# Kernel tuning notes

Hardware: AMD Instinct MI355X
Metric: run time of the kernel (lower is better)

## Reference

```python
import jax, jax.numpy as jnp
import numpy as np

NUM_CHUNKS = 8
TOP_K = 2
IN_F = 4096
HID_F = 4096
OUT_F = 4096
B = 4096


def setup_inputs() -> dict:
    key = jax.random.key(0)
    k = jax.random.split(key, 5)
    cin = IN_F // NUM_CHUNKS    # 512
    cout = HID_F // NUM_CHUNKS  # 512
    s_in = 1.0 / np.sqrt(cin)
    s_fin = 1.0 / np.sqrt(cout * TOP_K)
    return {
        "x": jax.random.normal(k[0], (B, IN_F), dtype=jnp.float32),
        # stacked chunk-expert Linear params: y = x @ W + b
        "W_chunks": jax.random.uniform(k[1], (NUM_CHUNKS, cin, cout), jnp.float32, -s_in, s_in),
        "b_chunks": jax.random.uniform(k[2], (NUM_CHUNKS, cout), jnp.float32, -s_in, s_in),
        "W_final": jax.random.uniform(k[3], (cout * TOP_K, OUT_F), jnp.float32, -s_fin, s_fin),
        "b_final": jax.random.uniform(k[4], (OUT_F,), jnp.float32, -s_fin, s_fin),
    }


def reference(x, W_chunks, b_chunks, W_final, b_final):
    Bsz = x.shape[0]
    # split into chunks along feature dim: (B, num_chunks, chunk_in)
    xr = x.reshape(Bsz, NUM_CHUNKS, -1)
    # per-chunk activity = mean(|chunk|) over the whole batch (matches torch .abs().mean())
    activities = jnp.mean(jnp.abs(xr), axis=(0, 2))  # (num_chunks,)
    _, topk_idx = jax.lax.top_k(activities, TOP_K)    # descending, like torch.topk
    # gather selected chunks and their expert weights, run small GEMMs
    x_sel = xr[:, topk_idx, :]                        # (B, k, chunk_in)
    h = jnp.einsum('bkc,kcd->bkd', x_sel, W_chunks[topk_idx]) + b_chunks[topk_idx]
    h = h.reshape(Bsz, -1)                            # concat along feature dim
    out = h @ W_final + b_final                       # (B, out_features)
    return out
```

## Files before the change

kernel.cpp:

```cpp
#include <hip/hip_runtime.h>


typedef __bf16 bf16x8_t __attribute__((ext_vector_type(8)));
typedef float  f32x4_t  __attribute__((ext_vector_type(4)));

__device__ inline unsigned short f2bf(float f) {
    __bf16 b = (__bf16)f;
    return __builtin_bit_cast(unsigned short, b);
}


__device__ inline void stage_glds(const unsigned short* gtile, int stride, int row0,
                                  unsigned short* lds, int lane) {
    const int r8 = lane >> 3;
    const int gg = (lane & 7) ^ r8;
    const unsigned short* gp = gtile + (size_t)(row0 + r8) * stride + gg * 8;
    unsigned short* lp = lds + row0 * 64;
    __builtin_amdgcn_global_load_lds((const __attribute__((address_space(1))) void*)gp,
                                     (__attribute__((address_space(3))) void*)lp,
                                     16, 0, 0);
}

__device__ inline bf16x8_t ldsfrag(const unsigned short* Ls, int row, int kb) {
    return *(const bf16x8_t*)(Ls + row * 64 + (((kb >> 3) ^ (row & 7)) * 8));
}

__global__ void activity_kernel(const float* __restrict__ x, float* __restrict__ part) {
    const int chunk = blockIdx.y;
    const int tid = threadIdx.x;
    const int colf4 = tid & 127;
    const int rsub = tid >> 7;
    const float4* base = (const float4*)x + (size_t)chunk * 128 + colf4;
    float s = 0.f;
    #pragma unroll 4
    for (int i = 0; i < 32; ++i) {
        int row = blockIdx.x * 64 + i * 2 + rsub;
        float4 v = base[(size_t)row * 1024];
        s += fabsf(v.x) + fabsf(v.y) + fabsf(v.z) + fabsf(v.w);
    }
    #pragma unroll
    for (int off = 32; off > 0; off >>= 1) s += __shfl_down(s, off, 64);
    __shared__ float wsum[4];
    if ((tid & 63) == 0) wsum[tid >> 6] = s;
    __syncthreads();
    if (tid == 0) part[chunk * 64 + blockIdx.x] = wsum[0] + wsum[1] + wsum[2] + wsum[3];
}

__global__ void topk_kernel(const float* __restrict__ part, int* __restrict__ idx) {
    __shared__ float act[8];
    const int lane = threadIdx.x & 63;
    const int wave = threadIdx.x >> 6;
    float s = part[wave * 64 + lane];
    #pragma unroll
    for (int off = 32; off > 0; off >>= 1) s += __shfl_down(s, off, 64);
    if (lane == 0) act[wave] = s;
    __syncthreads();
    if (threadIdx.x == 0) {
        float v0 = -1e30f, v1 = -1e30f; int b0 = 0, b1 = 0;
        for (int i = 0; i < 8; ++i) {
            float v = act[i];
            if (v > v0) { v1 = v0; b1 = b0; v0 = v; b0 = i; }
            else if (v > v1) { v1 = v; b1 = i; }
        }
        idx[0] = b0; idx[1] = b1;
    }
}

__global__ void transpose_cvt_kernel(const float* __restrict__ src, unsigned short* __restrict__ dst,
                                     int R, int C, const int* __restrict__ idx, int chunk_elems) {
    if (idx) { src += (size_t)idx[blockIdx.z] * chunk_elems; dst += (size_t)blockIdx.z * chunk_elems; }
    __shared__ float tile[32][33];
    const int tx = threadIdx.x, ty = threadIdx.y;
    const int cb = blockIdx.x * 32, rb = blockIdx.y * 32;
    #pragma unroll
    for (int i = 0; i < 4; ++i)
        tile[ty + i * 8][tx] = src[(size_t)(rb + ty + i * 8) * C + cb + tx];
    __syncthreads();
    #pragma unroll
    for (int i = 0; i < 4; ++i)
        dst[(size_t)(cb + ty + i * 8) * R + rb + tx] = f2bf(tile[tx][ty + i * 8]);
}

__global__ __launch_bounds__(256, 2)
void gemm1_kernel(const float* __restrict__ x, const unsigned short* __restrict__ wct,
                  const float* __restrict__ bc, const int* __restrict__ idx,
                  unsigned short* __restrict__ h) {
    const int z = blockIdx.z;
    const int idxz = idx[z];
    const int m0 = blockIdx.x * 64;
    const int n0 = blockIdx.y * 64;

    __shared__ unsigned short As[64 * 64];
    __shared__ unsigned short Bs[64 * 64];

    const int tid = threadIdx.x;
    const int wave = tid >> 6;
    const int lane = tid & 63;
    const int wm = (wave >> 1) * 32;
    const int wn = (wave & 1) * 32;
    const int rl = lane & 15;
    const int quad = lane >> 4;

    const float* xtile = x + (size_t)m0 * 4096 + idxz * 512;
    const unsigned short* bttile = wct + (size_t)z * 512 * 512 + (size_t)n0 * 512;

    f32x4_t acc[2][2] = {};

    const int ar = tid >> 2;
    const int aq = tid & 3;

    for (int k0 = 0; k0 < 512; k0 += 64) {
        #pragma unroll
        for (int s = wave; s < 8; s += 4)
            stage_glds(bttile + k0, 512, s * 8, Bs, lane);
        const float* gr = xtile + (size_t)ar * 4096 + k0;
        #pragma unroll
        for (int j = 0; j < 2; ++j) {
            int gg = aq * 2 + j;
            float4 a = *(const float4*)(gr + gg * 8);
            float4 b = *(const float4*)(gr + gg * 8 + 4);
            bf16x8_t v;
            v[0] = (__bf16)a.x; v[1] = (__bf16)a.y; v[2] = (__bf16)a.z; v[3] = (__bf16)a.w;
            v[4] = (__bf16)b.x; v[5] = (__bf16)b.y; v[6] = (__bf16)b.z; v[7] = (__bf16)b.w;
            *(bf16x8_t*)(As + ar * 64 + ((gg ^ (ar & 7)) * 8)) = v;
        }
        __syncthreads();
        #pragma unroll
        for (int kq = 0; kq < 2; ++kq) {
            const int kb = kq * 32 + quad * 8;
            bf16x8_t af[2], bfr[2];
            #pragma unroll
            for (int i = 0; i < 2; ++i) {
                af[i]  = ldsfrag(As, wm + i * 16 + rl, kb);
                bfr[i] = ldsfrag(Bs, wn + i * 16 + rl, kb);
            }
            #pragma unroll
            for (int mi = 0; mi < 2; ++mi)
                #pragma unroll
                for (int ni = 0; ni < 2; ++ni)
                    acc[mi][ni] = __builtin_amdgcn_mfma_f32_16x16x32_bf16(af[mi], bfr[ni], acc[mi][ni], 0, 0, 0);
        }
        __syncthreads();
    }

    const int row_l = quad * 4;
    const float* bias = bc + (size_t)idxz * 512;
    #pragma unroll
    for (int ni = 0; ni < 2; ++ni) {
        int col = n0 + wn + ni * 16 + rl;
        float bv = bias[col];
        #pragma unroll
        for (int mi = 0; mi < 2; ++mi) {
            #pragma unroll
            for (int j = 0; j < 4; ++j) {
                int row = m0 + wm + mi * 16 + row_l + j;
                h[(size_t)row * 1024 + z * 512 + col] = f2bf(acc[mi][ni][j] + bv);
            }
        }
    }
}

__global__ __launch_bounds__(256, 2)
void gemm2_kernel(const unsigned short* __restrict__ A, const unsigned short* __restrict__ Bt,
                  const float* __restrict__ bias, float* __restrict__ C) {
    const int m0 = blockIdx.x * 128;
    const int n0 = blockIdx.y * 128;

    __shared__ unsigned short As[128 * 64];
    __shared__ unsigned short Bs[128 * 64];

    const int tid = threadIdx.x;
    const int wave = tid >> 6;
    const int lane = tid & 63;
    const int wm = (wave >> 1) * 64;
    const int wn = (wave & 1) * 64;
    const int rl = lane & 15;
    const int quad = lane >> 4;

    const unsigned short* Atile = A + (size_t)m0 * 1024;
    const unsigned short* Btile = Bt + (size_t)n0 * 1024;

    f32x4_t acc[4][4] = {};

    for (int k0 = 0; k0 < 1024; k0 += 64) {
        #pragma unroll
        for (int s = wave; s < 32; s += 4) {
            if (s < 16) stage_glds(Atile + k0, 1024, s * 8, As, lane);
            else        stage_glds(Btile + k0, 1024, (s - 16) * 8, Bs, lane);
        }
        __syncthreads();
        #pragma unroll
        for (int kq = 0; kq < 2; ++kq) {
            const int kb = kq * 32 + quad * 8;
            bf16x8_t af[4], bfr[4];
            #pragma unroll
            for (int i = 0; i < 4; ++i) {
                af[i]  = ldsfrag(As, wm + i * 16 + rl, kb);
                bfr[i] = ldsfrag(Bs, wn + i * 16 + rl, kb);
            }
            #pragma unroll
            for (int mi = 0; mi < 4; ++mi)
                #pragma unroll
                for (int ni = 0; ni < 4; ++ni)
                    acc[mi][ni] = __builtin_amdgcn_mfma_f32_16x16x32_bf16(af[mi], bfr[ni], acc[mi][ni], 0, 0, 0);
        }
        __syncthreads();
    }

    const int row_l = quad * 4;
    float bv[4];
    #pragma unroll
    for (int ni = 0; ni < 4; ++ni) bv[ni] = bias[n0 + wn + ni * 16 + rl];
    #pragma unroll
    for (int mi = 0; mi < 4; ++mi) {
        #pragma unroll
        for (int ni = 0; ni < 4; ++ni) {
            int col = n0 + wn + ni * 16 + rl;
            #pragma unroll
            for (int j = 0; j < 4; ++j) {
                int row = m0 + wm + mi * 16 + row_l + j;
                C[(size_t)row * 4096 + col] = acc[mi][ni][j] + bv[ni];
            }
        }
    }
}

extern "C" void kernel_launch(void* const* d_in, const int* in_sizes, int n_in,
                              void* d_out, int out_size, void* d_ws, size_t ws_size,
                              hipStream_t stream) {
    const float* x    = (const float*)d_in[0];
    const float* Wc   = (const float*)d_in[1];
    const float* bc   = (const float*)d_in[2];
    const float* Wf   = (const float*)d_in[3];
    const float* bfin = (const float*)d_in[4];
    float* out = (float*)d_out;

    float* part = (float*)d_ws;
    int*   idx  = (int*)((char*)d_ws + 2048);
    unsigned short* h   = (unsigned short*)((char*)d_ws + 4096);
    unsigned short* wct = h   + (size_t)4096 * 1024;
    unsigned short* wft = wct + (size_t)2 * 512 * 512;

    activity_kernel<<<dim3(64, 8), 256, 0, stream>>>(x, part);
    topk_kernel<<<1, 512, 0, stream>>>(part, idx);
    transpose_cvt_kernel<<<dim3(16, 16, 2), dim3(32, 8), 0, stream>>>(Wc, wct, 512, 512, idx, 512 * 512);
    transpose_cvt_kernel<<<dim3(128, 32, 1), dim3(32, 8), 0, stream>>>(Wf, wft, 1024, 4096, nullptr, 0);

    gemm1_kernel<<<dim3(64, 8, 2), 256, 0, stream>>>(x, wct, bc, idx, h);
    gemm2_kernel<<<dim3(32, 32, 1), 256, 0, stream>>>(h, wft, bfin, out);
}
```

Measured before the change: 193.1 us.

## Fuse all stages into one cooperative persistent kernel with grid syncs

```diff
diff --git a/kernel.cpp b/kernel.cpp
--- a/kernel.cpp
+++ b/kernel.cpp
@@ -1,4 +1,7 @@
 #include <hip/hip_runtime.h>
+#include <hip/hip_cooperative_groups.h>
+
+namespace cg = cooperative_groups;
 
 
 typedef __bf16 bf16x8_t __attribute__((ext_vector_type(8)));
@@ -8,7 +11,6 @@
     __bf16 b = (__bf16)f;
     return __builtin_bit_cast(unsigned short, b);
 }
-
 
 __device__ inline void stage_glds(const unsigned short* gtile, int stride, int row0,
                                   unsigned short* lds, int lane) {
@@ -23,6 +25,248 @@
 
 __device__ inline bf16x8_t ldsfrag(const unsigned short* Ls, int row, int kb) {
     return *(const bf16x8_t*)(Ls + row * 64 + (((kb >> 3) ^ (row & 7)) * 8));
+}
+
+__device__ inline void gemm1_tile(const float* __restrict__ x, const unsigned short* __restrict__ wct,
+                                  const float* __restrict__ bc, unsigned short* __restrict__ h,
+                                  int z, int idxz, int m0, int n0,
+                                  unsigned short* As, unsigned short* Bs,
+                                  int tid, int wave, int lane) {
+    const int wm = (wave >> 1) * 32;
+    const int wn = (wave & 1) * 32;
+    const int rl = lane & 15;
+    const int quad = lane >> 4;
+    const float* xtile = x + (size_t)m0 * 4096 + idxz * 512;
+    const unsigned short* bttile = wct + (size_t)z * 262144 + (size_t)n0 * 512;
+
+    f32x4_t acc[2][2] = {};
+    const int ar = tid >> 2;
+    const int aq = tid & 3;
+
+    for (int k0 = 0; k0 < 512; k0 += 64) {
+        #pragma unroll
+        for (int s = wave; s < 8; s += 4)
+            stage_glds(bttile + k0, 512, s * 8, Bs, lane);
+        const float* gr = xtile + (size_t)ar * 4096 + k0;
+        #pragma unroll
+        for (int j = 0; j < 2; ++j) {
+            int gg = aq * 2 + j;
+            float4 a = *(const float4*)(gr + gg * 8);
+            float4 c = *(const float4*)(gr + gg * 8 + 4);
+            bf16x8_t v;
+            v[0] = (__bf16)a.x; v[1] = (__bf16)a.y; v[2] = (__bf16)a.z; v[3] = (__bf16)a.w;
+            v[4] = (__bf16)c.x; v[5] = (__bf16)c.y; v[6] = (__bf16)c.z; v[7] = (__bf16)c.w;
+            *(bf16x8_t*)(As + ar * 64 + ((gg ^ (ar & 7)) * 8)) = v;
+        }
+        __syncthreads();
+        #pragma unroll
+        for (int kq = 0; kq < 2; ++kq) {
+            const int kb = kq * 32 + quad * 8;
+            bf16x8_t af[2], bfr[2];
+            #pragma unroll
+            for (int i = 0; i < 2; ++i) {
+                af[i]  = ldsfrag(As, wm + i * 16 + rl, kb);
+                bfr[i] = ldsfrag(Bs, wn + i * 16 + rl, kb);
+            }
+            #pragma unroll
+            for (int mi = 0; mi < 2; ++mi)
+                #pragma unroll
+                for (int ni = 0; ni < 2; ++ni)
+                    acc[mi][ni] = __builtin_amdgcn_mfma_f32_16x16x32_bf16(af[mi], bfr[ni], acc[mi][ni], 0, 0, 0);
+        }
+        __syncthreads();
+    }
+
+    const int row_l = quad * 4;
+    const float* bias = bc + (size_t)idxz * 512;
+    #pragma unroll
+    for (int ni = 0; ni < 2; ++ni) {
+        int col = n0 + wn + ni * 16 + rl;
+        float bv = bias[col];
+        #pragma unroll
+        for (int mi = 0; mi < 2; ++mi) {
+            #pragma unroll
+            for (int j = 0; j < 4; ++j) {
+                int row = m0 + wm + mi * 16 + row_l + j;
+                h[(size_t)row * 1024 + z * 512 + col] = f2bf(acc[mi][ni][j] + bv);
+            }
+        }
+    }
+}
+
+__device__ inline void gemm2_tile(const unsigned short* __restrict__ h, const unsigned short* __restrict__ wft,
+                                  const float* __restrict__ bfin, float* __restrict__ out,
+                                  int m0, int n0, unsigned short* As, unsigned short* Bs,
+                                  int wave, int lane) {
+    const int wm = (wave >> 1) * 64;
+    const int wn = (wave & 1) * 64;
+    const int rl = lane & 15;
+    const int quad = lane >> 4;
+    const unsigned short* Atile = h + (size_t)m0 * 1024;
+    const unsigned short* Btile = wft + (size_t)n0 * 1024;
+
+    f32x4_t acc[4][4] = {};
+
+    for (int k0 = 0; k0 < 1024; k0 += 64) {
+        #pragma unroll
+        for (int s = wave; s < 32; s += 4) {
+            if (s < 16) stage_glds(Atile + k0, 1024, s * 8, As, lane);
+            else        stage_glds(Btile + k0, 1024, (s - 16) * 8, Bs, lane);
+        }
+        __syncthreads();
+        #pragma unroll
+        for (int kq = 0; kq < 2; ++kq) {
+            const int kb = kq * 32 + quad * 8;
+            bf16x8_t af[4], bfr[4];
+            #pragma unroll
+            for (int i = 0; i < 4; ++i) {
+                af[i]  = ldsfrag(As, wm + i * 16 + rl, kb);
+                bfr[i] = ldsfrag(Bs, wn + i * 16 + rl, kb);
+            }
+            #pragma unroll
+            for (int mi = 0; mi < 4; ++mi)
+                #pragma unroll
+                for (int ni = 0; ni < 4; ++ni)
+                    acc[mi][ni] = __builtin_amdgcn_mfma_f32_16x16x32_bf16(af[mi], bfr[ni], acc[mi][ni], 0, 0, 0);
+        }
+        __syncthreads();
+    }
+
+    const int row_l = quad * 4;
+    float bv[4];
+    #pragma unroll
+    for (int ni = 0; ni < 4; ++ni) bv[ni] = bfin[n0 + wn + ni * 16 + rl];
+    #pragma unroll
+    for (int mi = 0; mi < 4; ++mi) {
+        #pragma unroll
+        for (int ni = 0; ni < 4; ++ni) {
+            int col = n0 + wn + ni * 16 + rl;
+            #pragma unroll
+            for (int j = 0; j < 4; ++j) {
+                int row = m0 + wm + mi * 16 + row_l + j;
+                out[(size_t)row * 4096 + col] = acc[mi][ni][j] + bv[ni];
+            }
+        }
+    }
+}
+
+__global__ __launch_bounds__(256, 2)
+void mega_kernel(const float* __restrict__ x, const float* __restrict__ Wc,
+                 const float* __restrict__ bc, const float* __restrict__ Wf,
+                 const float* __restrict__ bfin, float* __restrict__ out,
+                 float* __restrict__ part, int* __restrict__ idxg,
+                 unsigned short* __restrict__ h, unsigned short* __restrict__ wct,
+                 unsigned short* __restrict__ wft) {
+    cg::grid_group grid = cg::this_grid();
+    __shared__ __align__(16) unsigned char lds_raw[32 * 1024];
+
+    const int b = blockIdx.x;
+    const int tid = threadIdx.x;
+    const int wave = tid >> 6;
+    const int lane = tid & 63;
+
+    {
+        const int chunk = b & 7;
+        const int rg = b >> 3;
+        const int colf4 = tid & 127;
+        const int rsub = tid >> 7;
+        const float4* base = (const float4*)x + (size_t)chunk * 128 + colf4;
+        float s = 0.f;
+        #pragma unroll 4
+        for (int i = 0; i < 32; ++i) {
+            int row = rg * 64 + i * 2 + rsub;
+            float4 v = base[(size_t)row * 1024];
+            s += fabsf(v.x) + fabsf(v.y) + fabsf(v.z) + fabsf(v.w);
+        }
+        #pragma unroll
+        for (int off = 32; off > 0; off >>= 1) s += __shfl_down(s, off, 64);
+        float* wsum = (float*)lds_raw;
+        if (lane == 0) wsum[wave] = s;
+        __syncthreads();
+        if (tid == 0) part[chunk * 64 + rg] = wsum[0] + wsum[1] + wsum[2] + wsum[3];
+    }
+    __threadfence();
+    grid.sync();
+
+    if (b == 0) {
+        float* red = (float*)lds_raw;
+        float* act8 = (float*)(lds_raw + 1024);
+        const int c = tid >> 5, j = tid & 31;
+        red[tid] = part[c * 64 + j] + part[c * 64 + j + 32];
+        __syncthreads();
+        if (tid < 8) {
+            float a = 0.f;
+            for (int k = 0; k < 32; ++k) a += red[tid * 32 + k];
+            act8[tid] = a;
+        }
+        __syncthreads();
+        if (tid == 0) {
+            float v0 = -1e30f, v1 = -1e30f; int b0 = 0, b1 = 0;
+            for (int i = 0; i < 8; ++i) {
+                float v = act8[i];
+                if (v > v0) { v1 = v0; b1 = b0; v0 = v; b0 = i; }
+                else if (v > v1) { v1 = v; b1 = i; }
+            }
+            idxg[0] = b0; idxg[1] = b1;
+        }
+    }
+    __threadfence();
+    grid.sync();
+
+    const int sel0 = ((volatile int*)idxg)[0];
+    const int sel1 = ((volatile int*)idxg)[1];
+
+    {
+        float (*tile)[33] = (float (*)[33])lds_raw;
+        const int tx = tid & 31, ty = tid >> 5;
+        for (int j = b; j < 4608; j += 512) {
+            const float* src; unsigned short* dst; int R, C, cb, rb;
+            if (j < 4096) {
+                src = Wf; dst = wft; R = 1024; C = 4096;
+                cb = (j & 127) * 32; rb = (j >> 7) * 32;
+            } else {
+                int jj = j - 4096;
+                int z = jj >> 8; int t = jj & 255;
+                src = Wc + (size_t)(z ? sel1 : sel0) * 262144;
+                dst = wct + (size_t)z * 262144;
+                R = 512; C = 512;
+                cb = (t & 15) * 32; rb = (t >> 4) * 32;
+            }
+            __syncthreads();
+            #pragma unroll
+            for (int i = 0; i < 4; ++i)
+                tile[ty + i * 8][tx] = src[(size_t)(rb + ty + i * 8) * C + cb + tx];
+            __syncthreads();
+            #pragma unroll
+            for (int i = 0; i < 4; ++i)
+                dst[(size_t)(cb + ty + i * 8) * R + rb + tx] = f2bf(tile[tx][ty + i * 8]);
+        }
+    }
+    __threadfence();
+    grid.sync();
+
+    {
+        unsigned short* As = (unsigned short*)lds_raw;
+        unsigned short* Bs = (unsigned short*)(lds_raw + 8192);
+        #pragma unroll
+        for (int t = b; t < 1024; t += 512) {
+            const int z = t >> 9;
+            const int tt = t & 511;
+            gemm1_tile(x, wct, bc, h, z, z ? sel1 : sel0,
+                       (tt >> 3) * 64, (tt & 7) * 64, As, Bs, tid, wave, lane);
+        }
+    }
+    __threadfence();
+    grid.sync();
+
+    {
+        unsigned short* As = (unsigned short*)lds_raw;
+        unsigned short* Bs = (unsigned short*)(lds_raw + 16384);
+        #pragma unroll
+        for (int t = b; t < 1024; t += 512)
+            gemm2_tile(h, wft, bfin, out, (t >> 5) * 128, (t & 31) * 128,
+                       As, Bs, wave, lane);
+    }
 }
 
 __global__ void activity_kernel(const float* __restrict__ x, float* __restrict__ part) {
@@ -85,144 +329,20 @@
 void gemm1_kernel(const float* __restrict__ x, const unsigned short* __restrict__ wct,
                   const float* __restrict__ bc, const int* __restrict__ idx,
                   unsigned short* __restrict__ h) {
+    __shared__ __align__(16) unsigned short As[64 * 64];
+    __shared__ __align__(16) unsigned short Bs[64 * 64];
     const int z = blockIdx.z;
-    const int idxz = idx[z];
-    const int m0 = blockIdx.x * 64;
-    const int n0 = blockIdx.y * 64;
-
-    __shared__ unsigned short As[64 * 64];
-    __shared__ unsigned short Bs[64 * 64];
-
-    const int tid = threadIdx.x;
-    const int wave = tid >> 6;
-    const int lane = tid & 63;
-    const int wm = (wave >> 1) * 32;
-    const int wn = (wave & 1) * 32;
-    const int rl = lane & 15;
-    const int quad = lane >> 4;
-
-    const float* xtile = x + (size_t)m0 * 4096 + idxz * 512;
-    const unsigned short* bttile = wct + (size_t)z * 512 * 512 + (size_t)n0 * 512;
-
-    f32x4_t acc[2][2] = {};
-
-    const int ar = tid >> 2;
-    const int aq = tid & 3;
-
-    for (int k0 = 0; k0 < 512; k0 += 64) {
-        #pragma unroll
-        for (int s = wave; s < 8; s += 4)
-            stage_glds(bttile + k0, 512, s * 8, Bs, lane);
-        const float* gr = xtile + (size_t)ar * 4096 + k0;
-        #pragma unroll
-        for (int j = 0; j < 2; ++j) {
-            int gg = aq * 2 + j;
-            float4 a = *(const float4*)(gr + gg * 8);
-            float4 b = *(const float4*)(gr + gg * 8 + 4);
-            bf16x8_t v;
-            v[0] = (__bf16)a.x; v[1] = (__bf16)a.y; v[2] = (__bf16)a.z; v[3] = (__bf16)a.w;
-            v[4] = (__bf16)b.x; v[5] = (__bf16)b.y; v[6] = (__bf16)b.z; v[7] = (__bf16)b.w;
-            *(bf16x8_t*)(As + ar * 64 + ((gg ^ (ar & 7)) * 8)) = v;
-        }
-        __syncthreads();
-        #pragma unroll
-        for (int kq = 0; kq < 2; ++kq) {
-            const int kb = kq * 32 + quad * 8;
-            bf16x8_t af[2], bfr[2];
-            #pragma unroll
-            for (int i = 0; i < 2; ++i) {
-                af[i]  = ldsfrag(As, wm + i * 16 + rl, kb);
-                bfr[i] = ldsfrag(Bs, wn + i * 16 + rl, kb);
-            }
-            #pragma unroll
-            for (int mi = 0; mi < 2; ++mi)
-                #pragma unroll
-                for (int ni = 0; ni < 2; ++ni)
-                    acc[mi][ni] = __builtin_amdgcn_mfma_f32_16x16x32_bf16(af[mi], bfr[ni], acc[mi][ni], 0, 0, 0);
-        }
-        __syncthreads();
-    }
-
-    const int row_l = quad * 4;
-    const float* bias = bc + (size_t)idxz * 512;
-    #pragma unroll
-    for (int ni = 0; ni < 2; ++ni) {
-        int col = n0 + wn + ni * 16 + rl;
-        float bv = bias[col];
-        #pragma unroll
-        for (int mi = 0; mi < 2; ++mi) {
-            #pragma unroll
-            for (int j = 0; j < 4; ++j) {
-                int row = m0 + wm + mi * 16 + row_l + j;
-                h[(size_t)row * 1024 + z * 512 + col] = f2bf(acc[mi][ni][j] + bv);
-            }
-        }
-    }
+    gemm1_tile(x, wct, bc, h, z, idx[z], blockIdx.x * 64, blockIdx.y * 64,
+               As, Bs, threadIdx.x, threadIdx.x >> 6, threadIdx.x & 63);
 }
 
 __global__ __launch_bounds__(256, 2)
-void gemm2_kernel(const unsigned short* __restrict__ A, const unsigned short* __restrict__ Bt,
-                  const float* __restrict__ bias, float* __restrict__ C) {
-    const int m0 = blockIdx.x * 128;
-    const int n0 = blockIdx.y * 128;
-
-    __shared__ unsigned short As[128 * 64];
-    __shared__ unsigned short Bs[128 * 64];
-
-    const int tid = threadIdx.x;
-    const int wave = tid >> 6;
-    const int lane = tid & 63;
-    const int wm = (wave >> 1) * 64;
-    const int wn = (wave & 1) * 64;
-    const int rl = lane & 15;
-    const int quad = lane >> 4;
-
-    const unsigned short* Atile = A + (size_t)m0 * 1024;
-    const unsigned short* Btile = Bt + (size_t)n0 * 1024;
-
-    f32x4_t acc[4][4] = {};
-
-    for (int k0 = 0; k0 < 1024; k0 += 64) {
-        #pragma unroll
-        for (int s = wave; s < 32; s += 4) {
-            if (s < 16) stage_glds(Atile + k0, 1024, s * 8, As, lane);
-            else        stage_glds(Btile + k0, 1024, (s - 16) * 8, Bs, lane);
-        }
-        __syncthreads();
-        #pragma unroll
-        for (int kq = 0; kq < 2; ++kq) {
-            const int kb = kq * 32 + quad * 8;
-            bf16x8_t af[4], bfr[4];
-            #pragma unroll
-            for (int i = 0; i < 4; ++i) {
-                af[i]  = ldsfrag(As, wm + i * 16 + rl, kb);
-                bfr[i] = ldsfrag(Bs, wn + i * 16 + rl, kb);
-            }
-            #pragma unroll
-            for (int mi = 0; mi < 4; ++mi)
-                #pragma unroll
-                for (int ni = 0; ni < 4; ++ni)
-                    acc[mi][ni] = __builtin_amdgcn_mfma_f32_16x16x32_bf16(af[mi], bfr[ni], acc[mi][ni], 0, 0, 0);
-        }
-        __syncthreads();
-    }
-
-    const int row_l = quad * 4;
-    float bv[4];
-    #pragma unroll
-    for (int ni = 0; ni < 4; ++ni) bv[ni] = bias[n0 + wn + ni * 16 + rl];
-    #pragma unroll
-    for (int mi = 0; mi < 4; ++mi) {
-        #pragma unroll
-        for (int ni = 0; ni < 4; ++ni) {
-            int col = n0 + wn + ni * 16 + rl;
-            #pragma unroll
-            for (int j = 0; j < 4; ++j) {
-                int row = m0 + wm + mi * 16 + row_l + j;
-                C[(size_t)row * 4096 + col] = acc[mi][ni][j] + bv[ni];
-            }
-        }
-    }
+void gemm2_kernel(const unsigned short* __restrict__ h, const unsigned short* __restrict__ wft,
+                  const float* __restrict__ bfin, float* __restrict__ out) {
+    __shared__ __align__(16) unsigned short As[128 * 64];
+    __shared__ __align__(16) unsigned short Bs[128 * 64];
+    gemm2_tile(h, wft, bfin, out, blockIdx.x * 128, blockIdx.y * 128,
+               As, Bs, threadIdx.x >> 6, threadIdx.x & 63);
 }
 
 extern "C" void kernel_launch(void* const* d_in, const int* in_sizes, int n_in,
@@ -236,16 +356,22 @@
     float* out = (float*)d_out;
 
     float* part = (float*)d_ws;
-    int*   idx  = (int*)((char*)d_ws + 2048);
-    unsigned short* h   = (unsigned short*)((char*)d_ws + 4096);
+    int*   idxg = (int*)((char*)d_ws + 4096);
+    unsigned short* h   = (unsigned short*)((char*)d_ws + 8192);
     unsigned short* wct = h   + (size_t)4096 * 1024;
     unsigned short* wft = wct + (size_t)2 * 512 * 512;
 
-    activity_kernel<<<dim3(64, 8), 256, 0, stream>>>(x, part);
-    topk_kernel<<<1, 512, 0, stream>>>(part, idx);
-    transpose_cvt_kernel<<<dim3(16, 16, 2), dim3(32, 8), 0, stream>>>(Wc, wct, 512, 512, idx, 512 * 512);
-    transpose_cvt_kernel<<<dim3(128, 32, 1), dim3(32, 8), 0, stream>>>(Wf, wft, 1024, 4096, nullptr, 0);
-
-    gemm1_kernel<<<dim3(64, 8, 2), 256, 0, stream>>>(x, wct, bc, idx, h);
-    gemm2_kernel<<<dim3(32, 32, 1), 256, 0, stream>>>(h, wft, bfin, out);
-}
+    void* args[] = { (void*)&x, (void*)&Wc, (void*)&bc, (void*)&Wf, (void*)&bfin,
+                     (void*)&out, (void*)&part, (void*)&idxg, (void*)&h,
+                     (void*)&wct, (void*)&wft };
+    hipError_t e = hipLaunchCooperativeKernel((const void*)mega_kernel, dim3(512),
+                                              dim3(256), args, 0, stream);
+    if (e != hipSuccess) {
+        activity_kernel<<<dim3(64, 8), 256, 0, stream>>>(x, part);
+        topk_kernel<<<1, 512, 0, stream>>>(part, idxg);
+        transpose_cvt_kernel<<<dim3(16, 16, 2), dim3(32, 8), 0, stream>>>(Wc, wct, 512, 512, idxg, 512 * 512);
+        transpose_cvt_kernel<<<dim3(128, 32, 1), dim3(32, 8), 0, stream>>>(Wf, wft, 1024, 4096, nullptr, 0);
+        gemm1_kernel<<<dim3(64, 8, 2), 256, 0, stream>>>(x, wct, bc, idxg, h);
+        gemm2_kernel<<<dim3(32, 32, 1), 256, 0, stream>>>(h, wft, bfin, out);
+    }
+}
```

Result: slower. 643.0 us (+233.0%).

## Fuse activity/top-k, merge prep kernels, pre-gather bf16 x, widen gemm1 tile

Applied to the files above, without the earlier changes.

```diff
diff --git a/kernel.cpp b/kernel.cpp
--- a/kernel.cpp
+++ b/kernel.cpp
@@ -8,7 +8,6 @@
     __bf16 b = (__bf16)f;
     return __builtin_bit_cast(unsigned short, b);
 }
-
 
 __device__ inline void stage_glds(const unsigned short* gtile, int stride, int row0,
                                   unsigned short* lds, int lane) {
@@ -25,8 +24,11 @@
     return *(const bf16x8_t*)(Ls + row * 64 + (((kb >> 3) ^ (row & 7)) * 8));
 }
 
-__global__ void activity_kernel(const float* __restrict__ x, float* __restrict__ part) {
-    const int chunk = blockIdx.y;
+__global__ void activity_topk_kernel(const float* __restrict__ x, float* __restrict__ act,
+                                     int* __restrict__ counter, int* __restrict__ idxg) {
+    const int b = blockIdx.x;
+    const int chunk = b & 7;
+    const int rg = b >> 3;
     const int tid = threadIdx.x;
     const int colf4 = tid & 127;
     const int rsub = tid >> 7;
@@ -34,7 +36,7 @@
     float s = 0.f;
     #pragma unroll 4
     for (int i = 0; i < 32; ++i) {
-        int row = blockIdx.x * 64 + i * 2 + rsub;
+        int row = rg * 64 + i * 2 + rsub;
         float4 v = base[(size_t)row * 1024];
         s += fabsf(v.x) + fabsf(v.y) + fabsf(v.z) + fabsf(v.w);
     }
@@ -43,35 +45,54 @@
     __shared__ float wsum[4];
     if ((tid & 63) == 0) wsum[tid >> 6] = s;
     __syncthreads();
-    if (tid == 0) part[chunk * 64 + blockIdx.x] = wsum[0] + wsum[1] + wsum[2] + wsum[3];
-}
-
-__global__ void topk_kernel(const float* __restrict__ part, int* __restrict__ idx) {
-    __shared__ float act[8];
-    const int lane = threadIdx.x & 63;
-    const int wave = threadIdx.x >> 6;
-    float s = part[wave * 64 + lane];
-    #pragma unroll
-    for (int off = 32; off > 0; off >>= 1) s += __shfl_down(s, off, 64);
-    if (lane == 0) act[wave] = s;
-    __syncthreads();
-    if (threadIdx.x == 0) {
-        float v0 = -1e30f, v1 = -1e30f; int b0 = 0, b1 = 0;
-        for (int i = 0; i < 8; ++i) {
-            float v = act[i];
-            if (v > v0) { v1 = v0; b1 = b0; v0 = v; b0 = i; }
-            else if (v > v1) { v1 = v; b1 = i; }
-        }
-        idx[0] = b0; idx[1] = b1;
-    }
-}
-
-__global__ void transpose_cvt_kernel(const float* __restrict__ src, unsigned short* __restrict__ dst,
-                                     int R, int C, const int* __restrict__ idx, int chunk_elems) {
-    if (idx) { src += (size_t)idx[blockIdx.z] * chunk_elems; dst += (size_t)blockIdx.z * chunk_elems; }
+    if (tid == 0) {
+        atomicAdd(&act[chunk], wsum[0] + wsum[1] + wsum[2] + wsum[3]);
+        __threadfence();
+        int old = atomicAdd(counter, 1);
+        if (old == gridDim.x - 1) {
+            float v0 = -1e30f, v1 = -1e30f; int b0 = 0, b1 = 0;
+            for (int i = 0; i < 8; ++i) {
+                float v = atomicAdd(&act[i], 0.0f);
+                if (v > v0) { v1 = v0; b1 = b0; v0 = v; b0 = i; }
+                else if (v > v1) { v1 = v; b1 = i; }
+            }
+            idxg[0] = b0; idxg[1] = b1;
+            __threadfence();
+        }
+    }
+}
+
+__global__ void prep_kernel(const float* __restrict__ x, const float* __restrict__ Wc,
+                            const float* __restrict__ Wf, const int* __restrict__ idxg,
+                            unsigned short* __restrict__ xsel, unsigned short* __restrict__ wct,
+                            unsigned short* __restrict__ wft) {
+    const int j = blockIdx.x;
+    const int tid = threadIdx.x;
+    if (j < 4096) {
+        const int c = tid * 4;
+        const int z = c >> 9;
+        const int sc = idxg[z] * 512 + (c & 511);
+        float4 v = *(const float4*)(x + (size_t)j * 4096 + sc);
+        ushort4 o;
+        o.x = f2bf(v.x); o.y = f2bf(v.y); o.z = f2bf(v.z); o.w = f2bf(v.w);
+        *(ushort4*)(xsel + (size_t)j * 1024 + c) = o;
+        return;
+    }
     __shared__ float tile[32][33];
-    const int tx = threadIdx.x, ty = threadIdx.y;
-    const int cb = blockIdx.x * 32, rb = blockIdx.y * 32;
+    const int tx = tid & 31, ty = tid >> 5;
+    const float* src; unsigned short* dst; int R, C, cb, rb;
+    if (j < 8192) {
+        int jj = j - 4096;
+        src = Wf; dst = wft; R = 1024; C = 4096;
+        cb = (jj & 127) * 32; rb = (jj >> 7) * 32;
+    } else {
+        int jj = j - 8192;
+        int z = jj >> 8, t = jj & 255;
+        src = Wc + (size_t)idxg[z] * 262144;
+        dst = wct + (size_t)z * 262144;
+        R = 512; C = 512;
+        cb = (t & 15) * 32; rb = (t >> 4) * 32;
+    }
     #pragma unroll
     for (int i = 0; i < 4; ++i)
         tile[ty + i * 8][tx] = src[(size_t)(rb + ty + i * 8) * C + cb + tx];
@@ -81,63 +102,48 @@
         dst[(size_t)(cb + ty + i * 8) * R + rb + tx] = f2bf(tile[tx][ty + i * 8]);
 }
 
-__global__ __launch_bounds__(256, 2)
-void gemm1_kernel(const float* __restrict__ x, const unsigned short* __restrict__ wct,
-                  const float* __restrict__ bc, const int* __restrict__ idx,
+__global__ __launch_bounds__(256, 4)
+void gemm1_kernel(const unsigned short* __restrict__ xsel, const unsigned short* __restrict__ wct,
+                  const float* __restrict__ bc, const int* __restrict__ idxg,
                   unsigned short* __restrict__ h) {
+    __shared__ __align__(16) unsigned short As[64 * 64];
+    __shared__ __align__(16) unsigned short Bs[128 * 64];
     const int z = blockIdx.z;
-    const int idxz = idx[z];
+    const int idxz = idxg[z];
     const int m0 = blockIdx.x * 64;
-    const int n0 = blockIdx.y * 64;
-
-    __shared__ unsigned short As[64 * 64];
-    __shared__ unsigned short Bs[64 * 64];
-
+    const int n0 = blockIdx.y * 128;
     const int tid = threadIdx.x;
     const int wave = tid >> 6;
     const int lane = tid & 63;
     const int wm = (wave >> 1) * 32;
-    const int wn = (wave & 1) * 32;
+    const int wn = (wave & 1) * 64;
     const int rl = lane & 15;
     const int quad = lane >> 4;
 
-    const float* xtile = x + (size_t)m0 * 4096 + idxz * 512;
-    const unsigned short* bttile = wct + (size_t)z * 512 * 512 + (size_t)n0 * 512;
-
-    f32x4_t acc[2][2] = {};
-
-    const int ar = tid >> 2;
-    const int aq = tid & 3;
+    const unsigned short* Atile = xsel + (size_t)m0 * 1024 + z * 512;
+    const unsigned short* Btile = wct + (size_t)z * 262144 + (size_t)n0 * 512;
+
+    f32x4_t acc[2][4] = {};
 
     for (int k0 = 0; k0 < 512; k0 += 64) {
         #pragma unroll
-        for (int s = wave; s < 8; s += 4)
-            stage_glds(bttile + k0, 512, s * 8, Bs, lane);
-        const float* gr = xtile + (size_t)ar * 4096 + k0;
-        #pragma unroll
-        for (int j = 0; j < 2; ++j) {
-            int gg = aq * 2 + j;
-            float4 a = *(const float4*)(gr + gg * 8);
-            float4 b = *(const float4*)(gr + gg * 8 + 4);
-            bf16x8_t v;
-            v[0] = (__bf16)a.x; v[1] = (__bf16)a.y; v[2] = (__bf16)a.z; v[3] = (__bf16)a.w;
-            v[4] = (__bf16)b.x; v[5] = (__bf16)b.y; v[6] = (__bf16)b.z; v[7] = (__bf16)b.w;
-            *(bf16x8_t*)(As + ar * 64 + ((gg ^ (ar & 7)) * 8)) = v;
+        for (int s = wave; s < 24; s += 4) {
+            if (s < 8) stage_glds(Atile + k0, 1024, s * 8, As, lane);
+            else       stage_glds(Btile + k0, 512, (s - 8) * 8, Bs, lane);
         }
         __syncthreads();
         #pragma unroll
         for (int kq = 0; kq < 2; ++kq) {
             const int kb = kq * 32 + quad * 8;
-            bf16x8_t af[2], bfr[2];
-            #pragma unroll
-            for (int i = 0; i < 2; ++i) {
-                af[i]  = ldsfrag(As, wm + i * 16 + rl, kb);
-                bfr[i] = ldsfrag(Bs, wn + i * 16 + rl, kb);
-            }
+            bf16x8_t af[2], bfr[4];
+            #pragma unroll
+            for (int i = 0; i < 2; ++i) af[i]  = ldsfrag(As, wm + i * 16 + rl, kb);
+            #pragma unroll
+            for (int i = 0; i < 4; ++i) bfr[i] = ldsfrag(Bs, wn + i * 16 + rl, kb);
             #pragma unroll
             for (int mi = 0; mi < 2; ++mi)
                 #pragma unroll
-                for (int ni = 0; ni < 2; ++ni)
+                for (int ni = 0; ni < 4; ++ni)
                     acc[mi][ni] = __builtin_amdgcn_mfma_f32_16x16x32_bf16(af[mi], bfr[ni], acc[mi][ni], 0, 0, 0);
         }
         __syncthreads();
@@ -146,7 +152,7 @@
     const int row_l = quad * 4;
     const float* bias = bc + (size_t)idxz * 512;
     #pragma unroll
-    for (int ni = 0; ni < 2; ++ni) {
+    for (int ni = 0; ni < 4; ++ni) {
         int col = n0 + wn + ni * 16 + rl;
         float bv = bias[col];
         #pragma unroll
@@ -160,15 +166,13 @@
     }
 }
 
-__global__ __launch_bounds__(256, 2)
-void gemm2_kernel(const unsigned short* __restrict__ A, const unsigned short* __restrict__ Bt,
-                  const float* __restrict__ bias, float* __restrict__ C) {
+__global__ __launch_bounds__(256, 3)
+void gemm2_kernel(const unsigned short* __restrict__ h, const unsigned short* __restrict__ wft,
+                  const float* __restrict__ bfin, float* __restrict__ out) {
+    __shared__ __align__(16) unsigned short As[128 * 64];
+    __shared__ __align__(16) unsigned short Bs[128 * 64];
     const int m0 = blockIdx.x * 128;
     const int n0 = blockIdx.y * 128;
-
-    __shared__ unsigned short As[128 * 64];
-    __shared__ unsigned short Bs[128 * 64];
-
     const int tid = threadIdx.x;
     const int wave = tid >> 6;
     const int lane = tid & 63;
@@ -177,8 +181,8 @@
     const int rl = lane & 15;
     const int quad = lane >> 4;
 
-    const unsigned short* Atile = A + (size_t)m0 * 1024;
-    const unsigned short* Btile = Bt + (size_t)n0 * 1024;
+    const unsigned short* Atile = h + (size_t)m0 * 1024;
+    const unsigned short* Btile = wft + (size_t)n0 * 1024;
 
     f32x4_t acc[4][4] = {};
 
@@ -210,7 +214,7 @@
     const int row_l = quad * 4;
     float bv[4];
     #pragma unroll
-    for (int ni = 0; ni < 4; ++ni) bv[ni] = bias[n0 + wn + ni * 16 + rl];
+    for (int ni = 0; ni < 4; ++ni) bv[ni] = bfin[n0 + wn + ni * 16 + rl];
     #pragma unroll
     for (int mi = 0; mi < 4; ++mi) {
         #pragma unroll
@@ -219,7 +223,7 @@
             #pragma unroll
             for (int j = 0; j < 4; ++j) {
                 int row = m0 + wm + mi * 16 + row_l + j;
-                C[(size_t)row * 4096 + col] = acc[mi][ni][j] + bv[ni];
+                out[(size_t)row * 4096 + col] = acc[mi][ni][j] + bv[ni];
             }
         }
     }
@@ -235,17 +239,18 @@
     const float* bfin = (const float*)d_in[4];
     float* out = (float*)d_out;
 
-    float* part = (float*)d_ws;
-    int*   idx  = (int*)((char*)d_ws + 2048);
-    unsigned short* h   = (unsigned short*)((char*)d_ws + 4096);
-    unsigned short* wct = h   + (size_t)4096 * 1024;
-    unsigned short* wft = wct + (size_t)2 * 512 * 512;
-
-    activity_kernel<<<dim3(64, 8), 256, 0, stream>>>(x, part);
-    topk_kernel<<<1, 512, 0, stream>>>(part, idx);
-    transpose_cvt_kernel<<<dim3(16, 16, 2), dim3(32, 8), 0, stream>>>(Wc, wct, 512, 512, idx, 512 * 512);
-    transpose_cvt_kernel<<<dim3(128, 32, 1), dim3(32, 8), 0, stream>>>(Wf, wft, 1024, 4096, nullptr, 0);
-
-    gemm1_kernel<<<dim3(64, 8, 2), 256, 0, stream>>>(x, wct, bc, idx, h);
+    float* act     = (float*)d_ws;
+    int*   counter = (int*)((char*)d_ws + 64);
+    int*   idxg    = (int*)((char*)d_ws + 128);
+    unsigned short* xsel = (unsigned short*)((char*)d_ws + 4096);
+    unsigned short* h    = xsel + (size_t)4096 * 1024;
+    unsigned short* wct  = h    + (size_t)4096 * 1024;
+    unsigned short* wft  = wct  + (size_t)2 * 512 * 512;
+
+    hipMemsetAsync(d_ws, 0, 128, stream);
+
+    activity_topk_kernel<<<512, 256, 0, stream>>>(x, act, counter, idxg);
+    prep_kernel<<<8704, 256, 0, stream>>>(x, Wc, Wf, idxg, xsel, wct, wft);
+    gemm1_kernel<<<dim3(64, 4, 2), 256, 0, stream>>>(xsel, wct, bc, idxg, h);
     gemm2_kernel<<<dim3(32, 32, 1), 256, 0, stream>>>(h, wft, bfin, out);
 }
```

Measured after the change: 215.7 us. 11.7% more time.
